# Kernel optimization log

Hardware: AMD Instinct MI355X
Metric: run time of the kernel (lower is better)

## Reference

```python
import jax, jax.numpy as jnp
import numpy as np

B, S, H = 4, 2048, 1024

def setup_inputs() -> dict:
    key = jax.random.key(0)
    ks = jax.random.split(key, 6)
    scale = 1.0 / np.sqrt(H)
    return {
        "query": jax.random.normal(ks[0], (B, S, H), dtype=jnp.float32),
        "key":   jax.random.normal(ks[1], (B, S, H), dtype=jnp.float32),
        "value": jax.random.normal(ks[2], (B, S, H), dtype=jnp.float32),
        "Wq": jax.random.normal(ks[3], (H, H), dtype=jnp.float32) * scale,
        "Wk": jax.random.normal(ks[4], (H, H), dtype=jnp.float32) * scale,
        "Wv": jax.random.normal(ks[5], (H, H), dtype=jnp.float32) * scale,
    }

def reference(query, key, value, Wq, Wk, Wv):
    # nn.Linear(bias=False): y = x @ W.T
    q = jnp.einsum('bsh,oh->bso', query, Wq)
    k = jnp.einsum('bsh,oh->bso', key, Wk)
    v = jnp.einsum('bsh,oh->bso', value, Wv)
    # full QK^T scores [B, Q, K], scaled by sqrt(hidden_size)
    scores = jnp.einsum('bqh,bkh->bqk', q, k) / jnp.sqrt(jnp.asarray(H, q.dtype))
    attn = jax.nn.softmax(scores, axis=2)
    return jnp.einsum('bqk,bkh->bqh', attn, v)
```

## Files before the change

kernel.cpp:

```cpp
#include <hip/hip_runtime.h>
#include <hip/hip_bf16.h>
#include <stdint.h>

#define BATCH 4
#define SLEN  2048
#define HID   1024

typedef __attribute__((ext_vector_type(8))) short bfrag8;
typedef __attribute__((ext_vector_type(4))) float facc4;
typedef __attribute__((ext_vector_type(4))) unsigned short us4;

__device__ __forceinline__ unsigned short f2b(float f) {
  union { float f; unsigned int i; } x; x.f = f;
  unsigned int r = x.i + 0x7FFFu + ((x.i >> 16) & 1u);
  return (unsigned short)(r >> 16);
}

__device__ __forceinline__ void gl_lds16(const void* g, void* l) {
  __builtin_amdgcn_global_load_lds(
      (const __attribute__((address_space(1))) void*)g,
      (__attribute__((address_space(3))) void*)l, 16, 0, 0);
}

__global__ __launch_bounds__(256) void cast_all(
    const float* __restrict__ q, const float* __restrict__ k,
    const float* __restrict__ v, const float* __restrict__ wq,
    const float* __restrict__ wk, const float* __restrict__ wv,
    us4* __restrict__ dst, float* __restrict__ lsum) {
  if (blockIdx.x < 8) {
    float4 z = {0.f, 0.f, 0.f, 0.f};
    ((float4*)lsum)[blockIdx.x * 256 + threadIdx.x] = z;
  }
  const long i = (long)blockIdx.x * 256 + threadIdx.x;
  const long S1 = 2097152, S2 = 4194304, S3 = 6291456,
             S4 = 6553600, S5 = 6815744;
  const float4* src; long off;
  if (i < S2) {
    if (i < S1) { src = (const float4*)q;  off = i; }
    else        { src = (const float4*)k;  off = i - S1; }
  } else if (i < S3) { src = (const float4*)v;  off = i - S2; }
  else if   (i < S4) { src = (const float4*)wq; off = i - S3; }
  else if   (i < S5) { src = (const float4*)wk; off = i - S4; }
  else               { src = (const float4*)wv; off = i - S5; }
  float4 x = src[off];
  us4 o;
  o.x = f2b(x.x); o.y = f2b(x.y); o.z = f2b(x.z); o.w = f2b(x.w);
  dst[i] = o;
}

template <int NT>
__device__ __forceinline__ void core256(
    const unsigned short* __restrict__ A, const unsigned short* __restrict__ B,
    const int lda, const int ldb,
    unsigned short* __restrict__ As, unsigned short* __restrict__ Bs,
    facc4 (&acc)[8][4]) {
  const int tid  = threadIdx.x;
  const int lane = tid & 63;
  const int wave = tid >> 6;
  const int wm = wave >> 2;
  const int wn = wave & 3;
  const int ln = lane & 15;
  const int lq = lane >> 4;
  const int swz = ln & 7;

  const int row0 = tid >> 3;
  const int blk  = (tid & 7) ^ (row0 & 7);
  const unsigned short* pA = A + (long)row0 * lda + blk * 8;
  const unsigned short* pB = B + (long)row0 * ldb + blk * 8;
  const long a64 = 64l * lda, b64 = 64l * ldb;
  unsigned short* dA = As + tid * 8;
  unsigned short* dB = Bs + tid * 8;

#define STG_A(h, b, t) do { const unsigned short* g_ = pA + (h) * (a64 * 2) + (long)(t) * 64; \
    gl_lds16(g_,       dA + (b) * 16384 + (h) * 8192); \
    gl_lds16(g_ + a64, dA + (b) * 16384 + (h) * 8192 + 4096); } while (0)
#define STG_B(h, b, t) do { const unsigned short* g_ = pB + (h) * (b64 * 2) + (long)(t) * 64; \
    gl_lds16(g_,       dB + (b) * 16384 + (h) * 8192); \
    gl_lds16(g_ + b64, dB + (b) * 16384 + (h) * 8192 + 4096); } while (0)

  const int o0 = (lq ^ swz) * 8;
  const int o1 = ((4 + lq) ^ swz) * 8;
  const int aOfs = wm * 8192 + ln * 64;
  const int bOfs = (wn >> 1) * 8192 + ((wn & 1) * 64 + ln) * 64;

#define RD_A4(dst, bufb, mb) do { \
  _Pragma("unroll") for (int m_ = 0; m_ < 4; ++m_) { \
    dst[m_][0] = *(const bfrag8*)(As + (bufb) + aOfs + ((mb) + m_) * 1024 + o0); \
    dst[m_][1] = *(const bfrag8*)(As + (bufb) + aOfs + ((mb) + m_) * 1024 + o1); \
  } } while (0)
#define RD_B2(dst, bufb, nb) do { \
  _Pragma("unroll") for (int n_ = 0; n_ < 2; ++n_) { \
    dst[n_][0] = *(const bfrag8*)(Bs + (bufb) + bOfs + ((nb) + n_) * 1024 + o0); \
    dst[n_][1] = *(const bfrag8*)(Bs + (bufb) + bOfs + ((nb) + n_) * 1024 + o1); \
  } } while (0)

#define MFMAQ(AF, BF, MO, NO) do { \
  _Pragma("unroll") for (int m_ = 0; m_ < 4; ++m_) \
  _Pragma("unroll") for (int n_ = 0; n_ < 2; ++n_) { \
    acc[(MO)+m_][(NO)+n_] = __builtin_amdgcn_mfma_f32_16x16x32_bf16( \
        AF[m_][0], BF[n_][0], acc[(MO)+m_][(NO)+n_], 0, 0, 0); \
    acc[(MO)+m_][(NO)+n_] = __builtin_amdgcn_mfma_f32_16x16x32_bf16( \
        AF[m_][1], BF[n_][1], acc[(MO)+m_][(NO)+n_], 0, 0, 0); \
  } } while (0)

#define PH_MID \
  __builtin_amdgcn_s_barrier(); \
  asm volatile("s_waitcnt lgkmcnt(0)" ::: "memory"); \
  __builtin_amdgcn_sched_barrier(0); \
  __builtin_amdgcn_s_setprio(1)
#define PH_END \
  __builtin_amdgcn_s_setprio(0); \
  __builtin_amdgcn_sched_barrier(0); \
  __builtin_amdgcn_s_barrier()

  STG_A(0, 0, 0); STG_A(1, 0, 0); STG_B(0, 0, 0); STG_B(1, 0, 0);
  STG_B(0, 1, 1); STG_B(1, 1, 1);
  asm volatile("s_waitcnt vmcnt(4)" ::: "memory");
  __builtin_amdgcn_s_barrier();

  constexpr int NI = NT / 2;
#pragma unroll 1
  for (int i = 0; i < NI - 1; ++i) {
    const int O1 = 2 * i + 1, E2 = 2 * i + 2, O2 = 2 * i + 3;
    {
      bfrag8 a0[4][2], a1[4][2], b0[2][2], b1[2][2];
      RD_A4(a0, 0, 0); RD_B2(b0, 0, 0); STG_A(0, 1, O1);
      PH_MID; MFMAQ(a0, b0, 0, 0); PH_END;
      RD_B2(b1, 0, 2); STG_A(1, 1, O1);
      PH_MID; MFMAQ(a0, b1, 0, 2); PH_END;
      RD_A4(a1, 0, 4); STG_B(0, 0, E2);
      PH_MID; MFMAQ(a1, b1, 4, 2); PH_END;
      STG_B(1, 0, E2);
      PH_MID; MFMAQ(a1, b0, 4, 0);
      __builtin_amdgcn_s_setprio(0);
      __builtin_amdgcn_sched_barrier(0);
      asm volatile("s_waitcnt vmcnt(4)" ::: "memory");
      __builtin_amdgcn_s_barrier();
    }
    {
      bfrag8 a0[4][2], a1[4][2], b0[2][2], b1[2][2];
      RD_A4(a0, 16384, 0); RD_B2(b0, 16384, 0); STG_A(0, 0, E2);
      PH_MID; MFMAQ(a0, b0, 0, 0); PH_END;
      RD_B2(b1, 16384, 2); STG_A(1, 0, E2);
      PH_MID; MFMAQ(a0, b1, 0, 2); PH_END;
      RD_A4(a1, 16384, 4); STG_B(0, 1, O2);
      PH_MID; MFMAQ(a1, b1, 4, 2); PH_END;
      STG_B(1, 1, O2);
      PH_MID; MFMAQ(a1, b0, 4, 0);
      __builtin_amdgcn_s_setprio(0);
      __builtin_amdgcn_sched_barrier(0);
      asm volatile("s_waitcnt vmcnt(4)" ::: "memory");
      __builtin_amdgcn_s_barrier();
    }
  }
  {
    const int O1 = NT - 1;
    {
      bfrag8 a0[4][2], a1[4][2], b0[2][2], b1[2][2];
      RD_A4(a0, 0, 0); RD_B2(b0, 0, 0); STG_A(0, 1, O1);
      PH_MID; MFMAQ(a0, b0, 0, 0); PH_END;
      RD_B2(b1, 0, 2); STG_A(1, 1, O1);
      PH_MID; MFMAQ(a0, b1, 0, 2); PH_END;
      RD_A4(a1, 0, 4);
      PH_MID; MFMAQ(a1, b1, 4, 2); PH_END;
      PH_MID; MFMAQ(a1, b0, 4, 0);
      __builtin_amdgcn_s_setprio(0);
      __builtin_amdgcn_sched_barrier(0);
      asm volatile("s_waitcnt vmcnt(0)" ::: "memory");
      __builtin_amdgcn_s_barrier();
    }
    {
      bfrag8 a0[4][2], a1[4][2], b0[2][2], b1[2][2];
      RD_A4(a0, 16384, 0); RD_B2(b0, 16384, 0);
      PH_MID; MFMAQ(a0, b0, 0, 0); PH_END;
      RD_B2(b1, 16384, 2);
      PH_MID; MFMAQ(a0, b1, 0, 2); PH_END;
      RD_A4(a1, 16384, 4);
      PH_MID; MFMAQ(a1, b1, 4, 2); PH_END;
      PH_MID; MFMAQ(a1, b0, 4, 0);
      __builtin_amdgcn_s_setprio(0);
    }
  }
#undef PH_MID
#undef PH_END
#undef MFMAQ
#undef RD_A4
#undef RD_B2
#undef STG_A
#undef STG_B
}

__global__ __launch_bounds__(512, 2) void proj3_256(
    const unsigned short* __restrict__ Xq, const unsigned short* __restrict__ Wqb,
    const unsigned short* __restrict__ Xk, const unsigned short* __restrict__ Wkb,
    const unsigned short* __restrict__ Xv, const unsigned short* __restrict__ Wvb,
    unsigned short* __restrict__ Qb, unsigned short* __restrict__ Kb,
    unsigned short* __restrict__ Vt) {
  extern __shared__ unsigned short smem[];
  unsigned short* As = smem;
  unsigned short* Bs = smem + 32768;

  const int pid = blockIdx.x;
  const int p2  = (pid & 7) * 48 + (pid >> 3);
  const int g   = p2 >> 7;
  const int within = p2 & 127;

  const unsigned short* A; const unsigned short* B; unsigned short* C;
  long bm, bn; int ldc_;
  if (g == 0)      { A = Xq;  B = Wqb; C = Qb; }
  else if (g == 1) { A = Xk;  B = Wkb; C = Kb; }
  else             { A = Wvb; B = Xv;  C = Vt; }
  if (g < 2) { bm = (long)(within >> 2) * 256; bn = (long)(within & 3)  * 256; ldc_ = 1024; }
  else       { bm = (long)(within >> 5) * 256; bn = (long)(within & 31) * 256; ldc_ = 8192; }

  facc4 acc[8][4] = {};
  core256<HID / 64>(A + bm * 1024, B + bn * 1024, 1024, 1024, As, Bs, acc);

  const int lane = threadIdx.x & 63, wave = threadIdx.x >> 6;
  const int wm = wave >> 2, wn = wave & 3;
  const int ln = lane & 15, lq = lane >> 4;
#pragma unroll
  for (int m = 0; m < 8; ++m)
#pragma unroll
    for (int n = 0; n < 4; ++n) {
      const long mm = bm + wm * 128 + m * 16 + lq * 4;
      const long nn = bn + wn * 64 + n * 16 + ln;
#pragma unroll
      for (int r = 0; r < 4; ++r)
        C[(mm + r) * (long)ldc_ + nn] = f2b(acc[m][n][r]);
    }
}

__global__ __launch_bounds__(512, 2) void scores256(
    const unsigned short* __restrict__ Q, const unsigned short* __restrict__ Kb,
    unsigned short* __restrict__ P, float* __restrict__ lsum) {
  extern __shared__ unsigned short smem[];
  unsigned short* As = smem;
  unsigned short* Bs = smem + 32768;

  const long z = blockIdx.z;
  const int pid = blockIdx.y * 8 + blockIdx.x;
  const int p2  = (pid & 7) * 8 + (pid >> 3);
  const long bm = (long)(p2 >> 3) * 256;
  const long bn = (long)(p2 & 7) * 256;

  const long SH = (long)SLEN * HID, SS = (long)SLEN * SLEN;
  facc4 acc[8][4] = {};
  core256<HID / 64>(Q + z * SH + bm * 1024, Kb + z * SH + bn * 1024, 1024, 1024,
                    As, Bs, acc);

  unsigned short* Pz = P + z * SS;
  float* lz = lsum + z * SLEN;
  const int lane = threadIdx.x & 63, wave = threadIdx.x >> 6;
  const int wm = wave >> 2, wn = wave & 3;
  const int ln = lane & 15, lq = lane >> 4;
#pragma unroll
  for (int m = 0; m < 8; ++m) {
#pragma unroll
    for (int r = 0; r < 4; ++r) {
      const long q = bm + wm * 128 + m * 16 + lq * 4 + r;
      float rowsum = 0.f;
#pragma unroll
      for (int n = 0; n < 4; ++n) {
        const long kcol = bn + wn * 64 + n * 16 + ln;
        float e = __expf(acc[m][n][r] * 0.03125f);
        Pz[q * (long)SLEN + kcol] = f2b(e);
        rowsum += e;
      }
      rowsum += __shfl_xor(rowsum, 1, 64);
      rowsum += __shfl_xor(rowsum, 2, 64);
      rowsum += __shfl_xor(rowsum, 4, 64);
      rowsum += __shfl_xor(rowsum, 8, 64);
      if (ln == 0) atomicAdd(&lz[q], rowsum);
    }
  }
}

template <int MODE, typename OutT>
__global__ __launch_bounds__(256) void gemm_nt(
    const unsigned short* __restrict__ A, const unsigned short* __restrict__ B,
    OutT* __restrict__ C, int K, int lda, int ldb, int ldc,
    long aStrideZ, long bStrideZ, long cStrideZ, float alpha,
    float* __restrict__ lsum) {
  A += (long)blockIdx.z * aStrideZ;
  B += (long)blockIdx.z * bStrideZ;
  C += (long)blockIdx.z * cStrideZ;
  const long lz = (long)blockIdx.z * SLEN;

  const int nbm = gridDim.x, nbn = gridDim.y;
  const int nb  = nbm * nbn;
  const int pid = blockIdx.y * nbm + blockIdx.x;
  const int p2  = (pid & 7) * (nb >> 3) + (pid >> 3);
  const int GROUP = 4;
  const int gsize = GROUP * nbn;
  const int gid   = p2 / gsize;
  const int rem   = p2 - gid * gsize;
  const long bm = (long)(gid * GROUP + (rem & (GROUP - 1))) * 128;
  const long bn = (long)(rem >> 2) * 128;

  __shared__ __align__(16) unsigned short As[128 * 64];
  __shared__ __align__(16) unsigned short Bs[128 * 64];

  const int tid  = threadIdx.x;
  const int lane = tid & 63;
  const int wave = tid >> 6;
  const int wr   = (wave >> 1) * 64;
  const int wc   = (wave & 1) * 64;
  const int ln   = lane & 15;
  const int lq   = lane >> 4;
  const int swz  = ln & 7;

  facc4 acc[4][4] = {};

  const unsigned short* ap[4]; const unsigned short* bp[4];
  unsigned short* asd[4]; unsigned short* bsd[4];
#pragma unroll
  for (int j = 0; j < 4; ++j) {
    const int c   = j * 256 + tid;
    const int row = c >> 3;
    const int src = ((c & 7) ^ (row & 7)) * 8;
    ap[j]  = A + (bm + row) * (long)lda + src;
    bp[j]  = B + (bn + row) * (long)ldb + src;
    asd[j] = &As[c * 8];
    bsd[j] = &Bs[c * 8];
  }

  for (int k0 = 0; k0 < K; k0 += 64) {
#pragma unroll
    for (int j = 0; j < 4; ++j) { gl_lds16(ap[j], asd[j]); ap[j] += 64; }
#pragma unroll
    for (int j = 0; j < 4; ++j) { gl_lds16(bp[j], bsd[j]); bp[j] += 64; }
    __syncthreads();

#pragma unroll
    for (int kk = 0; kk < 2; ++kk) {
      bfrag8 af[4], bfr[4];
#pragma unroll
      for (int i = 0; i < 4; ++i)
        af[i] = *(const bfrag8*)&As[(wr + i * 16 + ln) * 64 + ((kk * 4 + lq) ^ swz) * 8];
#pragma unroll
      for (int j = 0; j < 4; ++j)
        bfr[j] = *(const bfrag8*)&Bs[(wc + j * 16 + ln) * 64 + ((kk * 4 + lq) ^ swz) * 8];
#pragma unroll
      for (int i = 0; i < 4; ++i)
#pragma unroll
        for (int j = 0; j < 4; ++j)
          acc[i][j] = __builtin_amdgcn_mfma_f32_16x16x32_bf16(af[i], bfr[j], acc[i][j], 0, 0, 0);
    }
    __syncthreads();
  }

  if constexpr (MODE == 1) {
#pragma unroll
    for (int i = 0; i < 4; ++i) {
#pragma unroll
      for (int r = 0; r < 4; ++r) {
        const long m = bm + wr + i * 16 + lq * 4 + r;
        float rowsum = 0.f;
#pragma unroll
        for (int j = 0; j < 4; ++j) {
          const long n = bn + wc + j * 16 + ln;
          float e = __expf(acc[i][j][r] * alpha);
          C[m * (long)ldc + n] = (OutT)f2b(e);
          rowsum += e;
        }
        rowsum += __shfl_xor(rowsum, 1, 64);
        rowsum += __shfl_xor(rowsum, 2, 64);
        rowsum += __shfl_xor(rowsum, 4, 64);
        rowsum += __shfl_xor(rowsum, 8, 64);
        if (ln == 0) atomicAdd(&lsum[lz + m], rowsum);
      }
    }
  } else {
    float inv[16];
#pragma unroll
    for (int i = 0; i < 4; ++i)
#pragma unroll
      for (int r = 0; r < 4; ++r)
        inv[i * 4 + r] = 1.0f / lsum[lz + bm + wr + i * 16 + lq * 4 + r];
#pragma unroll
    for (int i = 0; i < 4; ++i)
#pragma unroll
      for (int j = 0; j < 4; ++j) {
        const long m = bm + wr + i * 16 + lq * 4;
        const long n = bn + wc + j * 16 + ln;
#pragma unroll
        for (int r = 0; r < 4; ++r)
          ((float*)C)[(m + r) * (long)ldc + n] = acc[i][j][r] * inv[i * 4 + r];
      }
  }
}

extern "C" void kernel_launch(void* const* d_in, const int* in_sizes, int n_in,
                              void* d_out, int out_size, void* d_ws, size_t ws_size,
                              hipStream_t stream) {
  const float* q_in = (const float*)d_in[0];
  const float* k_in = (const float*)d_in[1];
  const float* v_in = (const float*)d_in[2];
  const float* wq   = (const float*)d_in[3];
  const float* wk   = (const float*)d_in[4];
  const float* wv   = (const float*)d_in[5];
  float* out = (float*)d_out;

  const long NXH = (long)BATCH * SLEN * HID;
  const long NW  = (long)HID * HID;
  const long SH  = (long)SLEN * HID;
  const long SS  = (long)SLEN * SLEN;

  unsigned short* ws = (unsigned short*)d_ws;
  unsigned short* Xq  = ws;
  unsigned short* Xk  = Xq  + NXH;
  unsigned short* Xv  = Xk  + NXH;
  unsigned short* Wqb = Xv  + NXH;
  unsigned short* Wkb = Wqb + NW;
  unsigned short* Wvb = Wkb + NW;
  unsigned short* Qb  = Wvb + NW;
  unsigned short* Kb  = Qb  + NXH;
  unsigned short* Vt  = Kb  + NXH;
  float*          lsum = (float*)(Vt + NXH);
  unsigned short* P   = Xq;

  static bool attr_done = false;
  if (!attr_done) {
    hipFuncSetAttribute(reinterpret_cast<const void*>(proj3_256),
                        hipFuncAttributeMaxDynamicSharedMemorySize, 131072);
    hipFuncSetAttribute(reinterpret_cast<const void*>(scores256),
                        hipFuncAttributeMaxDynamicSharedMemorySize, 131072);
    attr_done = true;
  }

  cast_all<<<dim3(27648), dim3(256), 0, stream>>>(q_in, k_in, v_in, wq, wk, wv,
                                                  (us4*)ws, lsum);

  proj3_256<<<dim3(384), dim3(512), 131072, stream>>>(
      Xq, Wqb, Xk, Wkb, Xv, Wvb, Qb, Kb, Vt);

  scores256<<<dim3(8, 8, BATCH), dim3(512), 131072, stream>>>(Qb, Kb, P, lsum);

  gemm_nt<2, float><<<dim3(16, 8, BATCH), dim3(256), 0, stream>>>(
      P, Vt, out, SLEN, SLEN, BATCH * SLEN, HID, SS, SLEN, SH, 1.0f, lsum);
}
```

Baseline: 283.3 us.

## Replace 256x256 projection GEMM with simpler 128x128-tile kernel using more blocks

The QKV projection switches from the 256x256-tile, 512-thread pipelined core256 kernel (384 blocks, 128KB dynamic LDS) to a new 128x128-tile, 256-thread kernel with static 32KB LDS, launched as 1536 blocks with a grouped tile ordering. The goal is better occupancy and load balance across the CUs (384 blocks is a poor fit for the CU count). In exchange it loses the software-pipelined, priority-scheduled inner loop and has lower data reuse per tile. The new loop is single-buffered, with a barrier on each iteration.

```diff
diff --git a/kernel.cpp b/kernel.cpp
--- a/kernel.cpp
+++ b/kernel.cpp
@@ -46,6 +46,98 @@
   us4 o;
   o.x = f2b(x.x); o.y = f2b(x.y); o.z = f2b(x.z); o.w = f2b(x.w);
   dst[i] = o;
+}
+
+__global__ __launch_bounds__(256) void proj3(
+    const unsigned short* __restrict__ Xq, const unsigned short* __restrict__ Wqb,
+    const unsigned short* __restrict__ Xk, const unsigned short* __restrict__ Wkb,
+    const unsigned short* __restrict__ Xv, const unsigned short* __restrict__ Wvb,
+    unsigned short* __restrict__ Qb, unsigned short* __restrict__ Kb,
+    unsigned short* __restrict__ Vt) {
+  const int pid = blockIdx.x;
+  const int p2     = (pid & 7) * 192 + (pid >> 3);
+  const int g      = p2 >> 9;
+  const int within = p2 & 511;
+
+  const unsigned short* A; const unsigned short* B; unsigned short* C;
+  long bm, bn; int ldc_;
+  if (g == 0)      { A = Xq; B = Wqb; C = Qb; }
+  else if (g == 1) { A = Xk; B = Wkb; C = Kb; }
+  else             { A = Wvb; B = Xv; C = Vt; }
+  if (g < 2) {
+    const int gid = within >> 5, rem = within & 31;
+    bm = (long)(gid * 4 + (rem & 3)) * 128;
+    bn = (long)(rem >> 2) * 128;
+    ldc_ = 1024;
+  } else {
+    const int gid = within >> 8, rem = within & 255;
+    bm = (long)(gid * 4 + (rem & 3)) * 128;
+    bn = (long)(rem >> 2) * 128;
+    ldc_ = 8192;
+  }
+
+  __shared__ __align__(16) unsigned short As[128 * 64];
+  __shared__ __align__(16) unsigned short Bs[128 * 64];
+
+  const int tid  = threadIdx.x;
+  const int lane = tid & 63;
+  const int wave = tid >> 6;
+  const int wr   = (wave >> 1) * 64;
+  const int wc   = (wave & 1) * 64;
+  const int ln   = lane & 15;
+  const int lq   = lane >> 4;
+  const int swz  = ln & 7;
+
+  facc4 acc[4][4] = {};
+
+  const unsigned short* ap[4]; const unsigned short* bp[4];
+  unsigned short* asd[4]; unsigned short* bsd[4];
+#pragma unroll
+  for (int j = 0; j < 4; ++j) {
+    const int c   = j * 256 + tid;
+    const int row = c >> 3;
+    const int src = ((c & 7) ^ (row & 7)) * 8;
+    ap[j]  = A + (bm + row) * 1024 + src;
+    bp[j]  = B + (bn + row) * 1024 + src;
+    asd[j] = &As[c * 8];
+    bsd[j] = &Bs[c * 8];
+  }
+
+  for (int k0 = 0; k0 < 1024; k0 += 64) {
+#pragma unroll
+    for (int j = 0; j < 4; ++j) { gl_lds16(ap[j], asd[j]); ap[j] += 64; }
+#pragma unroll
+    for (int j = 0; j < 4; ++j) { gl_lds16(bp[j], bsd[j]); bp[j] += 64; }
+    __syncthreads();
+
+#pragma unroll
+    for (int kk = 0; kk < 2; ++kk) {
+      bfrag8 af[4], bfr[4];
+#pragma unroll
+      for (int i = 0; i < 4; ++i)
+        af[i] = *(const bfrag8*)&As[(wr + i * 16 + ln) * 64 + ((kk * 4 + lq) ^ swz) * 8];
+#pragma unroll
+      for (int j = 0; j < 4; ++j)
+        bfr[j] = *(const bfrag8*)&Bs[(wc + j * 16 + ln) * 64 + ((kk * 4 + lq) ^ swz) * 8];
+#pragma unroll
+      for (int i = 0; i < 4; ++i)
+#pragma unroll
+        for (int j = 0; j < 4; ++j)
+          acc[i][j] = __builtin_amdgcn_mfma_f32_16x16x32_bf16(af[i], bfr[j], acc[i][j], 0, 0, 0);
+    }
+    __syncthreads();
+  }
+
+#pragma unroll
+  for (int i = 0; i < 4; ++i)
+#pragma unroll
+    for (int j = 0; j < 4; ++j) {
+      const long m = bm + wr + i * 16 + lq * 4;
+      const long n = bn + wc + j * 16 + ln;
+#pragma unroll
+      for (int r = 0; r < 4; ++r)
+        C[(m + r) * (long)ldc_ + n] = f2b(acc[i][j][r]);
+    }
 }
 
 template <int NT>
@@ -190,47 +282,6 @@
 #undef STG_B
 }
 
-__global__ __launch_bounds__(512, 2) void proj3_256(
-    const unsigned short* __restrict__ Xq, const unsigned short* __restrict__ Wqb,
-    const unsigned short* __restrict__ Xk, const unsigned short* __restrict__ Wkb,
-    const unsigned short* __restrict__ Xv, const unsigned short* __restrict__ Wvb,
-    unsigned short* __restrict__ Qb, unsigned short* __restrict__ Kb,
-    unsigned short* __restrict__ Vt) {
-  extern __shared__ unsigned short smem[];
-  unsigned short* As = smem;
-  unsigned short* Bs = smem + 32768;
-
-  const int pid = blockIdx.x;
-  const int p2  = (pid & 7) * 48 + (pid >> 3);
-  const int g   = p2 >> 7;
-  const int within = p2 & 127;
-
-  const unsigned short* A; const unsigned short* B; unsigned short* C;
-  long bm, bn; int ldc_;
-  if (g == 0)      { A = Xq;  B = Wqb; C = Qb; }
-  else if (g == 1) { A = Xk;  B = Wkb; C = Kb; }
-  else             { A = Wvb; B = Xv;  C = Vt; }
-  if (g < 2) { bm = (long)(within >> 2) * 256; bn = (long)(within & 3)  * 256; ldc_ = 1024; }
-  else       { bm = (long)(within >> 5) * 256; bn = (long)(within & 31) * 256; ldc_ = 8192; }
-
-  facc4 acc[8][4] = {};
-  core256<HID / 64>(A + bm * 1024, B + bn * 1024, 1024, 1024, As, Bs, acc);
-
-  const int lane = threadIdx.x & 63, wave = threadIdx.x >> 6;
-  const int wm = wave >> 2, wn = wave & 3;
-  const int ln = lane & 15, lq = lane >> 4;
-#pragma unroll
-  for (int m = 0; m < 8; ++m)
-#pragma unroll
-    for (int n = 0; n < 4; ++n) {
-      const long mm = bm + wm * 128 + m * 16 + lq * 4;
-      const long nn = bn + wn * 64 + n * 16 + ln;
-#pragma unroll
-      for (int r = 0; r < 4; ++r)
-        C[(mm + r) * (long)ldc_ + nn] = f2b(acc[m][n][r]);
-    }
-}
-
 __global__ __launch_bounds__(512, 2) void scores256(
     const unsigned short* __restrict__ Q, const unsigned short* __restrict__ Kb,
     unsigned short* __restrict__ P, float* __restrict__ lsum) {
@@ -422,8 +473,6 @@
 
   static bool attr_done = false;
   if (!attr_done) {
-    hipFuncSetAttribute(reinterpret_cast<const void*>(proj3_256),
-                        hipFuncAttributeMaxDynamicSharedMemorySize, 131072);
     hipFuncSetAttribute(reinterpret_cast<const void*>(scores256),
                         hipFuncAttributeMaxDynamicSharedMemorySize, 131072);
     attr_done = true;
@@ -432,8 +481,8 @@
   cast_all<<<dim3(27648), dim3(256), 0, stream>>>(q_in, k_in, v_in, wq, wk, wv,
                                                   (us4*)ws, lsum);
 
-  proj3_256<<<dim3(384), dim3(512), 131072, stream>>>(
-      Xq, Wqb, Xk, Wkb, Xv, Wvb, Qb, Kb, Vt);
+  proj3<<<dim3(1536), dim3(256), 0, stream>>>(Xq, Wqb, Xk, Wkb, Xv, Wvb,
+                                              Qb, Kb, Vt);
 
   scores256<<<dim3(8, 8, BATCH), dim3(512), 131072, stream>>>(Qb, Kb, P, lsum);
 
```

Measured after the change: 277.7 us. 1.02x faster.
